# Optimization experiments

Hardware: AMD Instinct MI355X
Metric: run time of the kernel (lower is better)

## Reference

```python
import jax, jax.numpy as jnp
import numpy as np

D_MODEL = 512
NUM_HEADS = 8
D_K = D_MODEL // NUM_HEADS  # 64
NUM_FEATURES = 256
EPS = 1e-6


def _ortho_gaussian(m, d, seed):
    """Orthogonal random features: stacked QR blocks, rows rescaled to chi(d) norms."""
    rng = np.random.default_rng(seed)
    blocks = []
    for _ in range(int(np.ceil(m / d))):
        q, _ = np.linalg.qr(rng.standard_normal((d, d)))
        blocks.append(q.T)
    omega = np.concatenate(blocks, axis=0)[:m]
    norms = np.linalg.norm(rng.standard_normal((m, d)), axis=1)
    return (omega * norms[:, None]).astype(np.float32)


def setup_inputs() -> dict:
    key = jax.random.key(0)
    ks = jax.random.split(key, 7)
    B, L = 4, 8192
    s = 1.0 / np.sqrt(D_MODEL)
    return {
        "Q": jax.random.normal(ks[0], (B, L, D_MODEL), jnp.float32),
        "K": jax.random.normal(ks[1], (B, L, D_MODEL), jnp.float32),
        "V": jax.random.normal(ks[2], (B, L, D_MODEL), jnp.float32),
        "Wq": jax.random.normal(ks[3], (D_MODEL, D_MODEL), jnp.float32) * s,
        "Wk": jax.random.normal(ks[4], (D_MODEL, D_MODEL), jnp.float32) * s,
        "Wv": jax.random.normal(ks[5], (D_MODEL, D_MODEL), jnp.float32) * s,
        "Wo": jax.random.normal(ks[6], (D_MODEL, D_MODEL), jnp.float32) * s,
        "omega": jnp.asarray(_ortho_gaussian(NUM_FEATURES, D_K, 42)),
    }


def _phi(x, omega):
    """FAVOR+ positive softmax-kernel features. x: [B,H,L,d], omega: [m,d] -> [B,H,L,m]."""
    x = x * (D_K ** -0.25)  # fold in 1/sqrt(d_k) softmax scaling
    proj = jnp.einsum('bhld,md->bhlm', x, omega)
    sq = 0.5 * jnp.sum(x * x, axis=-1, keepdims=True)
    # subtract per-position max over features for numerical stability
    stab = jnp.max(proj, axis=-1, keepdims=True)
    return jnp.exp(proj - sq - stab) * (NUM_FEATURES ** -0.5) + EPS


def _split_heads(x, W):
    B, L, _ = x.shape
    return (x @ W).reshape(B, L, NUM_HEADS, D_K).transpose(0, 2, 1, 3)  # [B,H,L,d]


def reference(Q, K, V, Wq, Wk, Wv, Wo, omega):
    q = _split_heads(Q, Wq)
    k = _split_heads(K, Wk)
    v = _split_heads(V, Wv)
    qp = _phi(q, omega)  # [B,H,L,m]
    kp = _phi(k, omega)  # [B,H,L,m]
    # linear attention: O(L*m*d) instead of O(L^2)
    kv = jnp.einsum('bhlm,bhld->bhmd', kp, v)           # [B,H,m,d]
    num = jnp.einsum('bhlm,bhmd->bhld', qp, kv)          # [B,H,L,d]
    ksum = jnp.sum(kp, axis=2)                            # [B,H,m]
    den = jnp.einsum('bhlm,bhm->bhl', qp, ksum)          # [B,H,L]
    out = num / (den[..., None] + EPS)
    B, H, L, d = out.shape
    out = out.transpose(0, 2, 1, 3).reshape(B, L, H * d)
    return out @ Wo
```

## Files before the change

kernel.cpp:

```cpp
#include <hip/hip_runtime.h>

typedef unsigned int u32;
typedef __attribute__((ext_vector_type(8))) short short8;
typedef __attribute__((ext_vector_type(4))) short short4v;
typedef __attribute__((ext_vector_type(2))) u32 u32x2;
typedef __attribute__((ext_vector_type(4))) float f32x4;

#define DM 512
#define NH 8
#define DK 64
#define NF 256
#define L_ 8192
#define SCALE 0.35355339059327373f
#define INVSQM 0.0625f
#define EPS_ 1e-6f

__device__ __forceinline__ float bf2f(short s){
  union { u32 u; float f; } x; x.u = ((u32)(unsigned short)s) << 16; return x.f;
}
__device__ __forceinline__ short f2bf(float f){
  union { float f; u32 u; } x; x.f = f;
  u32 r = (x.u + 0x7FFF + ((x.u >> 16) & 1)) >> 16;
  return (short)r;
}
__device__ __forceinline__ u32 cvtpk(float lo, float hi){
  u32 r;
  asm("v_cvt_pk_bf16_f32 %0, %1, %2" : "=v"(r) : "v"(lo), "v"(hi));
  return r;
}

typedef const __attribute__((address_space(1))) u32* gas_t;
typedef __attribute__((address_space(3))) u32* las_t;
__device__ __forceinline__ void gl_lds16(const void* g, void* l){
  __builtin_amdgcn_global_load_lds((gas_t)g, (las_t)l, 16, 0, 0);
}
__device__ __forceinline__ f32x4 mfma16(short8 a, short8 b, f32x4 c){
  return __builtin_amdgcn_mfma_f32_16x16x32_bf16(a, b, c, 0, 0, 0);
}
__device__ __forceinline__ short8 lds_read8(const void* base, int byteoff){
  return *reinterpret_cast<const short8*>((const char*)base + byteoff);
}

__global__ __launch_bounds__(256) void k_wt(const float* __restrict__ W0, const float* __restrict__ W1,
                                            const float* __restrict__ W2, const float* __restrict__ W3,
                                            short* __restrict__ Wt){
  int bid = blockIdx.x;
  int mat = bid >> 6;
  int tr = (bid >> 3) & 7, tc = bid & 7;
  const float* W = mat==0 ? W0 : mat==1 ? W1 : mat==2 ? W2 : W3;
  short* O = Wt + (size_t)mat*DM*DM;
  __shared__ __align__(16) short tl[64*72];
  int t = threadIdx.x;
  #pragma unroll
  for (int i=0;i<4;++i){
    int c = i*256 + t;
    int r = c >> 4, cc = c & 15;
    f32x4 v = *reinterpret_cast<const f32x4*>(W + (size_t)(tr*64+r)*DM + tc*64 + cc*4);
    u32x2 o; o[0] = cvtpk(v[0], v[1]); o[1] = cvtpk(v[2], v[3]);
    *reinterpret_cast<u32x2*>((char*)tl + r*144 + cc*8) = o;
  }
  __syncthreads();
  #pragma unroll
  for (int i=0;i<2;++i){
    int c = i*256 + t;
    int n = c >> 3, kc = c & 7;
    short8 v;
    #pragma unroll
    for (int q=0;q<8;++q) v[q] = tl[(kc*8+q)*72 + n];
    *reinterpret_cast<short8*>(O + (size_t)(tc*64+n)*DM + tr*64 + kc*8) = v;
  }
}

__global__ __launch_bounds__(256) void k_omc(const float* __restrict__ Om, short* __restrict__ omc){
  int i = blockIdx.x*256 + threadIdx.x;
  f32x4 v = *((const f32x4*)Om + i);
  u32x2 o; o[0] = cvtpk(v[0], v[1]); o[1] = cvtpk(v[2], v[3]);
  *((u32x2*)omc + i) = o;
}

__global__ __launch_bounds__(256) void k_gemm3(const float* __restrict__ Q, const float* __restrict__ K,
                                               const float* __restrict__ V, const short* __restrict__ wt,
                                               short* __restrict__ qh, short* __restrict__ kh,
                                               short* __restrict__ vT, int rbase){
  __shared__ __align__(16) char smem[34816];
  short* lA = (short*)smem;
  short* lB = (short*)(smem + 16384);
  short* lC = (short*)smem;
  const int mode = blockIdx.y;
  const float* A = mode==0 ? Q : mode==1 ? K : V;
  const short* Bt = wt + (size_t)mode*DM*DM;
  const int t = threadIdx.x;
  const int w = t >> 6, lane = t & 63;
  const int wr = w >> 1, wc = w & 1;
  const int bid = blockIdx.x;
  const int bmx = gridDim.x >> 5;
  const int j = bid >> 3;
  const int bm = (bid & 7)*bmx + (j >> 2);
  const int bn = j & 3;
  const int row0 = bm*128, n0 = bn*128;
  f32x4 acc[4][4] = {};
  for (int ks=0; ks<8; ++ks){
    const float* gA32 = A + (size_t)(rbase+row0)*DM + ks*64;
    #pragma unroll
    for (int rnd=0; rnd<8; ++rnd){
      int c = rnd*256 + t;
      int r = c >> 4, cc = c & 15;
      f32x4 v = *reinterpret_cast<const f32x4*>(gA32 + (size_t)r*DM + cc*4);
      u32x2 o; o[0] = cvtpk(v[0], v[1]); o[1] = cvtpk(v[2], v[3]);
      int po = cc*8;
      *reinterpret_cast<u32x2*>((char*)lA + r*128 + (po ^ ((r&7)<<4))) = o;
    }
    const char* gB = (const char*)(Bt + (size_t)n0*DM + ks*64);
    #pragma unroll
    for (int rnd=0; rnd<4; ++rnd){
      int d = (rnd*256 + t)*16;
      int r = d >> 7, po = d & 127;
      gl_lds16(gB + (size_t)r*(DM*2) + (po ^ ((r&7)<<4)), (char*)lB + rnd*4096 + w*1024);
    }
    __syncthreads();
    #pragma unroll
    for (int kk=0; kk<2; ++kk){
      int kb = (kk*32 + ((lane>>4)<<3))*2;
      short8 af[4], bfr[4];
      #pragma unroll
      for (int i=0;i<4;++i){
        int m = wr*64 + i*16 + (lane&15);
        af[i] = lds_read8(lA, m*128 + (kb ^ ((m&7)<<4)));
      }
      #pragma unroll
      for (int j2=0;j2<4;++j2){
        int n = wc*64 + j2*16 + (lane&15);
        bfr[j2] = lds_read8(lB, n*128 + (kb ^ ((n&7)<<4)));
      }
      #pragma unroll
      for (int i=0;i<4;++i)
        #pragma unroll
        for (int j2=0;j2<4;++j2)
          acc[i][j2] = mfma16(af[i], bfr[j2], acc[i][j2]);
    }
    __syncthreads();
  }
  #pragma unroll
  for (int i=0;i<4;++i)
    #pragma unroll
    for (int j2=0;j2<4;++j2)
      #pragma unroll
      for (int jj=0;jj<4;++jj){
        int row = wr*64 + i*16 + ((lane>>4)<<2) + jj;
        int col = wc*64 + j2*16 + (lane&15);
        lC[row*136 + col] = f2bf(acc[i][j2][jj]);
      }
  __syncthreads();
  const int b = row0 >> 13;
  const int l0 = row0 & 8191;
  if (mode < 2){
    short* Os = mode ? kh : qh;
    #pragma unroll
    for (int it=0; it<8; ++it){
      int p = it*256 + t;
      int row = p >> 4, c16 = p & 15;
      short8 v = *reinterpret_cast<const short8*>((char*)lC + row*272 + c16*16);
      int col0 = n0 + c16*8;
      int h = col0 >> 6, dv = col0 & 63;
      size_t off = ((size_t)(b*NH + h)*L_ + (l0+row))*DK + dv;
      *reinterpret_cast<short8*>(Os + off) = v;
    }
  } else {
    #pragma unroll
    for (int it=0; it<8; ++it){
      int p = it*256 + t;
      int col = p >> 4, lp = p & 15;
      short8 v;
      #pragma unroll
      for (int q=0;q<8;++q) v[q] = lC[(lp*8+q)*136 + col];
      int h = (n0+col) >> 6, dv = (n0+col) & 63;
      size_t off = ((size_t)(b*NH+h)*DK + dv)*L_ + l0 + lp*8;
      *reinterpret_cast<short8*>(vT + off) = v;
    }
  }
}

__global__ __launch_bounds__(256) void k_gemmO(const short* __restrict__ A, const short* __restrict__ Bt,
                                               float* __restrict__ Out, int rbase){
  __shared__ __align__(16) short lA[128*64];
  __shared__ __align__(16) short lB[128*64];
  const int t = threadIdx.x;
  const int w = t >> 6, lane = t & 63;
  const int wr = w >> 1, wc = w & 1;
  const int bid = blockIdx.x;
  const int bmx = gridDim.x >> 5;
  const int j = bid >> 3;
  const int bm = (bid & 7)*bmx + (j >> 2);
  const int bn = j & 3;
  const int row0 = bm*128, n0 = bn*128;
  f32x4 acc[4][4] = {};
  for (int ks=0; ks<8; ++ks){
    const char* gA = (const char*)(A + (size_t)(rbase+row0)*DM + ks*64);
    #pragma unroll
    for (int rnd=0; rnd<4; ++rnd){
      int d = (rnd*256 + t)*16;
      int r = d >> 7, po = d & 127;
      gl_lds16(gA + (size_t)r*(DM*2) + (po ^ ((r&7)<<4)), (char*)lA + rnd*4096 + w*1024);
    }
    const char* gB = (const char*)(Bt + (size_t)n0*DM + ks*64);
    #pragma unroll
    for (int rnd=0; rnd<4; ++rnd){
      int d = (rnd*256 + t)*16;
      int r = d >> 7, po = d & 127;
      gl_lds16(gB + (size_t)r*(DM*2) + (po ^ ((r&7)<<4)), (char*)lB + rnd*4096 + w*1024);
    }
    __syncthreads();
    #pragma unroll
    for (int kk=0; kk<2; ++kk){
      int kb = (kk*32 + ((lane>>4)<<3))*2;
      short8 af[4], bfr[4];
      #pragma unroll
      for (int i=0;i<4;++i){
        int m = wr*64 + i*16 + (lane&15);
        af[i] = lds_read8(lA, m*128 + (kb ^ ((m&7)<<4)));
      }
      #pragma unroll
      for (int j2=0;j2<4;++j2){
        int n = wc*64 + j2*16 + (lane&15);
        bfr[j2] = lds_read8(lB, n*128 + (kb ^ ((n&7)<<4)));
      }
      #pragma unroll
      for (int i=0;i<4;++i)
        #pragma unroll
        for (int j2=0;j2<4;++j2)
          acc[i][j2] = mfma16(af[i], bfr[j2], acc[i][j2]);
    }
    __syncthreads();
  }
  #pragma unroll
  for (int i=0;i<4;++i)
    #pragma unroll
    for (int j2=0;j2<4;++j2)
      #pragma unroll
      for (int jj=0;jj<4;++jj){
        int row = wr*64 + i*16 + ((lane>>4)<<2) + jj;
        int col = wc*64 + j2*16 + (lane&15);
        Out[(size_t)(row0+row)*DM + n0 + col] = acc[i][j2][jj];
      }
}

__global__ __launch_bounds__(512) void k_phik(const short* __restrict__ kh, const short* __restrict__ vT,
                                              const short* __restrict__ omega,
                                              float* __restrict__ kvp, float* __restrict__ ksp){
  __shared__ __align__(16) short lOm[256*64];
  __shared__ __align__(16) short lK[128*64];
  __shared__ __align__(16) short lV[64*128];
  __shared__ __align__(16) short lP[256*136];
  __shared__ float lSq[128];
  __shared__ float lKsP[8][256];
  const int t = threadIdx.x, w = t>>6, lane = t&63;
  const int bid = blockIdx.x;
  const int bh = bid >> 3, sp = bid & 7;
  const char* khb = (const char*)(kh + (size_t)bh*L_*DK);
  const char* vtb = (const char*)(vT + (size_t)bh*DK*L_);
  #pragma unroll
  for (int rnd=0; rnd<4; ++rnd){
    int d = (rnd*512 + t)*16;
    int r = d >> 7, po = d & 127;
    gl_lds16((const char*)omega + r*128 + (po ^ ((r&7)<<4)), (char*)lOm + rnd*8192 + w*1024);
  }
  f32x4 kv[4][2] = {};
  float ksa[16] = {};
  for (int c=0;c<8;++c){
    int l0 = sp*1024 + c*128;
    #pragma unroll
    for (int rnd=0; rnd<2; ++rnd){
      int d = (rnd*512 + t)*16;
      { int r = d>>7, po = d&127;
        gl_lds16(khb + (size_t)(l0+r)*128 + (po ^ ((r&7)<<4)), (char*)lK + rnd*8192 + w*1024); }
      { int r = d>>8, po = d&255;
        gl_lds16(vtb + (size_t)r*(L_*2) + (size_t)l0*2 + (po ^ ((r&15)<<4)), (char*)lV + rnd*8192 + w*1024); }
    }
    __syncthreads();
    {
      int row = t >> 2, part = t & 3;
      float ss = 0.f;
      #pragma unroll
      for (int hh=0; hh<2; ++hh){
        int cb = part*32 + hh*16;
        short8 v = lds_read8(lK, row*128 + (cb ^ ((row&7)<<4)));
        #pragma unroll
        for (int q=0;q<8;++q){ float f = bf2f(v[q]); ss += f*f; }
      }
      ss += __shfl_xor(ss, 1, 64);
      ss += __shfl_xor(ss, 2, 64);
      if (part==0) lSq[row] = 0.0625f * ss;
    }
    __syncthreads();
    f32x4 p[16] = {};
    #pragma unroll
    for (int kk=0;kk<2;++kk){
      int kb = (kk*32 + ((lane>>4)<<3))*2;
      int m = w*16 + (lane&15);
      short8 a = lds_read8(lK, m*128 + (kb ^ ((m&7)<<4)));
      #pragma unroll
      for (int ft=0; ft<16; ++ft){
        int n = ft*16 + (lane&15);
        short8 b = lds_read8(lOm, n*128 + (kb ^ ((n&7)<<4)));
        p[ft] = mfma16(a, b, p[ft]);
      }
    }
    float mj[4] = {-1e30f,-1e30f,-1e30f,-1e30f};
    #pragma unroll
    for (int ft=0; ft<16; ++ft)
      #pragma unroll
      for (int j=0;j<4;++j){ float pv = p[ft][j]*SCALE; p[ft][j]=pv; mj[j] = fmaxf(mj[j], pv); }
    #pragma unroll
    for (int j=0;j<4;++j){
      float v = mj[j];
      v = fmaxf(v, __shfl_xor(v,1,64)); v = fmaxf(v, __shfl_xor(v,2,64));
      v = fmaxf(v, __shfl_xor(v,4,64)); v = fmaxf(v, __shfl_xor(v,8,64));
      mj[j] = v;
    }
    float sqv[4];
    #pragma unroll
    for (int j=0;j<4;++j) sqv[j] = lSq[w*16 + ((lane>>4)<<2) + j];
    int llb = w*16 + ((lane>>4)<<2);
    #pragma unroll
    for (int ft=0; ft<16; ++ft){
      int feat = ft*16 + (lane&15);
      float e0, e1, e2, e3;
      {
        e0 = __expf(p[ft][0] - sqv[0] - mj[0]) * INVSQM + EPS_;
        e1 = __expf(p[ft][1] - sqv[1] - mj[1]) * INVSQM + EPS_;
        e2 = __expf(p[ft][2] - sqv[2] - mj[2]) * INVSQM + EPS_;
        e3 = __expf(p[ft][3] - sqv[3] - mj[3]) * INVSQM + EPS_;
      }
      ksa[ft] += (e0 + e1) + (e2 + e3);
      u32x2 pk; pk[0] = cvtpk(e0, e1); pk[1] = cvtpk(e2, e3);
      *reinterpret_cast<u32x2*>((char*)lP + feat*272 + llb*2) = pk;
    }
    __syncthreads();
    #pragma unroll
    for (int ks2=0; ks2<4; ++ks2){
      int kb = (ks2*32 + ((lane>>4)<<3))*2;
      short8 a[4], b[2];
      #pragma unroll
      for (int i=0;i<4;++i){
        int m = i*16 + (lane&15);
        a[i] = lds_read8(lV, m*256 + (kb ^ ((m&15)<<4)));
      }
      #pragma unroll
      for (int j=0;j<2;++j){
        int n = (2*w+j)*16 + (lane&15);
        b[j] = lds_read8(lP, n*272 + kb);
      }
      #pragma unroll
      for (int i=0;i<4;++i)
        #pragma unroll
        for (int j=0;j<2;++j)
          kv[i][j] = mfma16(a[i], b[j], kv[i][j]);
    }
    __syncthreads();
  }
  float* kvb = kvp + (size_t)bid*64*256;
  #pragma unroll
  for (int i=0;i<4;++i)
    #pragma unroll
    for (int j=0;j<2;++j)
      #pragma unroll
      for (int jj=0;jj<4;++jj){
        int dv = i*16 + ((lane>>4)<<2) + jj;
        int feat = (2*w+j)*16 + (lane&15);
        kvb[dv*256 + feat] = kv[i][j][jj];
      }
  #pragma unroll
  for (int ft=0; ft<16; ++ft){
    float v = ksa[ft];
    v += __shfl_xor(v, 16, 64);
    v += __shfl_xor(v, 32, 64);
    if (lane < 16) lKsP[w][ft*16 + lane] = v;
  }
  __syncthreads();
  if (t < 256){
    float s = 0.f;
    #pragma unroll
    for (int wv=0; wv<8; ++wv) s += lKsP[wv][t];
    ksp[(size_t)bid*256 + t] = s;
  }
}

__global__ __launch_bounds__(256) void k_red(const float* __restrict__ kvp, const float* __restrict__ ksp,
                                             short* __restrict__ kvb, float* __restrict__ ksum){
  int bid = blockIdx.x;
  int bh = bid >> 3, part = bid & 7;
  int t = threadIdx.x;
  const float* base = kvp + (size_t)bh*8*16384;
  short* ob = kvb + (size_t)bh*16384;
  for (int i=0;i<8;++i){
    int e = part*2048 + i*256 + t;
    float s = 0.f;
    #pragma unroll
    for (int sp2=0; sp2<8; ++sp2) s += base[(size_t)sp2*16384 + e];
    ob[e] = f2bf(s);
  }
  if (part == 0){
    const float* kb = ksp + (size_t)bh*8*256;
    float s2 = 0.f;
    #pragma unroll
    for (int sp2=0; sp2<8; ++sp2) s2 += kb[sp2*256 + t];
    ksum[bh*256 + t] = s2;
  }
}

__global__ __launch_bounds__(512, 4) void k_phiq(const short* __restrict__ qh, const short* __restrict__ kvb,
                                                 const float* __restrict__ ksum, const short* __restrict__ omega,
                                                 short* __restrict__ attn){
  __shared__ __align__(16) char smem[69632];
  short* bufA = (short*)smem;
  short* bufB = (short*)(smem + 32768);
  float* lSq  = (float*)(smem + 67584);
  float* lKs  = (float*)(smem + 68096);
  float* lDen = (float*)(smem + 69120);
  const int t = threadIdx.x, w = t>>6, lane = t&63;
  const int bid = blockIdx.x;
  const int bh = bid >> 6, lt = bid & 63;
  const int l0 = lt*128;
  const char* qb = (const char*)(qh + (size_t)bh*L_*DK);
  #pragma unroll
  for (int rnd=0; rnd<4; ++rnd){
    int d = (rnd*512 + t)*16;
    int r = d>>7, po = d&127;
    gl_lds16((const char*)omega + r*128 + (po ^ ((r&7)<<4)), (char*)bufA + rnd*8192 + w*1024);
  }
  #pragma unroll
  for (int rnd=0; rnd<2; ++rnd){
    int d = (rnd*512 + t)*16;
    int r = d>>7, po = d&127;
    gl_lds16(qb + (size_t)(l0+r)*128 + (po ^ ((r&7)<<4)), (char*)bufB + rnd*8192 + w*1024);
  }
  if (t < 256) lKs[t] = ksum[bh*256 + t];
  __syncthreads();
  {
    int row = t >> 2, part = t & 3;
    float ss = 0.f;
    #pragma unroll
    for (int hh=0; hh<2; ++hh){
      int cb = part*32 + hh*16;
      short8 v = lds_read8(bufB, row*128 + (cb ^ ((row&7)<<4)));
      #pragma unroll
      for (int q=0;q<8;++q){ float f = bf2f(v[q]); ss += f*f; }
    }
    ss += __shfl_xor(ss, 1, 64);
    ss += __shfl_xor(ss, 2, 64);
    if (part==0) lSq[row] = 0.0625f * ss;
  }
  __syncthreads();
  f32x4 p[16] = {};
  #pragma unroll
  for (int kk=0;kk<2;++kk){
    int kb = (kk*32 + ((lane>>4)<<3))*2;
    int m = w*16 + (lane&15);
    short8 a = lds_read8(bufB, m*128 + (kb ^ ((m&7)<<4)));
    #pragma unroll
    for (int ft=0; ft<16; ++ft){
      int n = ft*16 + (lane&15);
      short8 b = lds_read8(bufA, n*128 + (kb ^ ((n&7)<<4)));
      p[ft] = mfma16(a, b, p[ft]);
    }
  }
  float mj[4] = {-1e30f,-1e30f,-1e30f,-1e30f};
  #pragma unroll
  for (int ft=0;ft<16;++ft)
    #pragma unroll
    for (int j=0;j<4;++j){ float pv = p[ft][j]*SCALE; p[ft][j]=pv; mj[j]=fmaxf(mj[j],pv); }
  #pragma unroll
  for (int j=0;j<4;++j){
    float v = mj[j];
    v = fmaxf(v,__shfl_xor(v,1,64)); v = fmaxf(v,__shfl_xor(v,2,64));
    v = fmaxf(v,__shfl_xor(v,4,64)); v = fmaxf(v,__shfl_xor(v,8,64));
    mj[j] = v;
  }
  float sqv[4];
  #pragma unroll
  for (int j=0;j<4;++j) sqv[j] = lSq[w*16 + ((lane>>4)<<2) + j];
  __syncthreads();
  const char* kvg = (const char*)(kvb + (size_t)bh*16384);
  #pragma unroll
  for (int rnd=0; rnd<4; ++rnd){
    int d = (rnd*512 + t)*16;
    int r = d>>9, po = d&511;
    gl_lds16(kvg + (size_t)r*512 + (po ^ ((r&31)<<4)), (char*)bufA + rnd*8192 + w*1024);
  }
  float dpart[4] = {0.f,0.f,0.f,0.f};
  const int rb = w*16 + ((lane>>4)<<2);
  #pragma unroll
  for (int ft=0;ft<8;++ft){
    int feat = ft*16 + (lane&15);
    float ksf = lKs[feat];
    #pragma unroll
    for (int j=0;j<4;++j){
      float e = __expf(p[ft][j]-sqv[j]-mj[j])*INVSQM + EPS_;
      dpart[j] += e*ksf;
      bufB[(rb+j)*136 + feat] = f2bf(e);
    }
  }
  __syncthreads();
  f32x4 nc[4] = {};
  #pragma unroll
  for (int ks2=0; ks2<4; ++ks2){
    int kb = (ks2*32 + ((lane>>4)<<3))*2;
    int n = w*16 + (lane&15);
    short8 bfr = lds_read8(bufB, n*272 + kb);
    #pragma unroll
    for (int i=0;i<4;++i){
      int mi = i*16 + (lane&15);
      short8 a = lds_read8(bufA, mi*512 + (kb ^ ((mi&31)<<4)));
      nc[i] = mfma16(a, bfr, nc[i]);
    }
  }
  #pragma unroll
  for (int ft=8;ft<16;++ft){
    int feat = ft*16 + (lane&15);
    float ksf = lKs[feat];
    #pragma unroll
    for (int j=0;j<4;++j){
      float e = __expf(p[ft][j]-sqv[j]-mj[j])*INVSQM + EPS_;
      dpart[j] += e*ksf;
      bufB[(rb+j)*136 + (feat-128)] = f2bf(e);
    }
  }
  #pragma unroll
  for (int j=0;j<4;++j){
    float v = dpart[j];
    v += __shfl_xor(v,1,64); v += __shfl_xor(v,2,64);
    v += __shfl_xor(v,4,64); v += __shfl_xor(v,8,64);
    if ((lane&15)==0) lDen[rb + j] = v;
  }
  #pragma unroll
  for (int ks2=4; ks2<8; ++ks2){
    int kbt = (ks2*32 + ((lane>>4)<<3))*2;
    int n = w*16 + (lane&15);
    short8 bfr = lds_read8(bufB, n*272 + (kbt - 256));
    #pragma unroll
    for (int i=0;i<4;++i){
      int mi = i*16 + (lane&15);
      short8 a = lds_read8(bufA, mi*512 + (kbt ^ ((mi&31)<<4)));
      nc[i] = mfma16(a, bfr, nc[i]);
    }
  }
  const int b = bh >> 3, h = bh & 7;
  const int l = w*16 + (lane&15);
  float rden = 1.0f / (lDen[l] + EPS_);
  #pragma unroll
  for (int i=0;i<4;++i){
    u32x2 ov;
    ov[0] = cvtpk(nc[i][0]*rden, nc[i][1]*rden);
    ov[1] = cvtpk(nc[i][2]*rden, nc[i][3]*rden);
    size_t off = ((size_t)(b*L_ + l0 + l))*DM + h*DK + i*16 + ((lane>>4)<<2);
    *reinterpret_cast<u32x2*>(attn + off) = ov;
  }
}

extern "C" void kernel_launch(void* const* d_in, const int* in_sizes, int n_in,
                              void* d_out, int out_size, void* d_ws, size_t ws_size,
                              hipStream_t stream){
  const float* Q  = (const float*)d_in[0];
  const float* K  = (const float*)d_in[1];
  const float* V  = (const float*)d_in[2];
  const float* Wq = (const float*)d_in[3];
  const float* Wk = (const float*)d_in[4];
  const float* Wv = (const float*)d_in[5];
  const float* Wo = (const float*)d_in[6];
  const float* Om = (const float*)d_in[7];
  char* ws = (char*)d_ws;

  short* wt  = (short*)(ws);
  short* omc = (short*)(ws + 2097152);

  k_wt<<<256, 256, 0, stream>>>(Wq, Wk, Wv, Wo, wt);
  k_omc<<<16, 256, 0, stream>>>(Om, omc);

  const size_t MONO_NEED = 120946688ull;
  if (ws_size >= MONO_NEED){
    short* qh   = (short*)(ws + 2162688);
    short* kh   = (short*)(ws + 35717120);
    short* vT   = (short*)(ws + 69271552);
    float* kvp  = (float*)(ws + 102825984);
    float* ksp  = (float*)(ws + 119603200);
    short* kvb  = (short*)(ws + 119865344);
    float* ksum = (float*)(ws + 120913920);
    short* attn = kh;
    k_gemm3<<<dim3(1024,3), 256, 0, stream>>>(Q, K, V, wt, qh, kh, vT, 0);
    k_phik<<<256, 512, 0, stream>>>(kh, vT, omc, kvp, ksp);
    k_red<<<256, 256, 0, stream>>>(kvp, ksp, kvb, ksum);
    k_phiq<<<2048, 512, 0, stream>>>(qh, kvb, ksum, omc, attn);
    k_gemmO<<<1024, 256, 0, stream>>>(attn, wt + 786432, (float*)d_out, 0);
  } else {
    short* qh   = (short*)(ws + 2162688);
    short* kh   = (short*)(ws + 10551296);
    short* vT   = (short*)(ws + 18939904);
    float* kvp  = (float*)(ws + 27328512);
    float* ksp  = (float*)(ws + 31522816);
    short* kvb  = (short*)(ws + 31588352);
    float* ksum = (float*)(ws + 31850496);
    short* attn = kh;
    for (int b=0; b<4; ++b){
      int rbase = b*8192;
      k_gemm3<<<dim3(256,3), 256, 0, stream>>>(Q, K, V, wt, qh, kh, vT, rbase);
      k_phik<<<64, 512, 0, stream>>>(kh, vT, omc, kvp, ksp);
      k_red<<<64, 256, 0, stream>>>(kvp, ksp, kvb, ksum);
      k_phiq<<<512, 512, 0, stream>>>(qh, kvb, ksum, omc, attn);
      k_gemmO<<<256, 256, 0, stream>>>(attn, wt + 786432,
                                       (float*)d_out + (size_t)b*8192*DM, 0);
    }
  }
}
```

Before: 269.7 us.

## Widen QKV projection tile to 128x256 to halve fp32 A reloads

The fused Q/K/V projection GEMM now computes a 128x256 output tile per block instead of 128x128, so each block converts and stages the fp32 activation tile once for twice as many output columns. The grid is halved, B staging doubles, accumulators double to 128 floats per thread, and the epilogue writes the two 128-column halves in sequence through a separate LDS region. The aim is to halve the redundant global reads and bf16 conversion of the large fp32 inputs. The cost is higher register and LDS use, which may lower occupancy, and fewer blocks in flight.

```diff
diff --git a/kernel.cpp b/kernel.cpp
--- a/kernel.cpp
+++ b/kernel.cpp
@@ -82,10 +82,10 @@
                                                const float* __restrict__ V, const short* __restrict__ wt,
                                                short* __restrict__ qh, short* __restrict__ kh,
                                                short* __restrict__ vT, int rbase){
-  __shared__ __align__(16) char smem[34816];
+  __shared__ __align__(16) char smem[51200];
   short* lA = (short*)smem;
   short* lB = (short*)(smem + 16384);
-  short* lC = (short*)smem;
+  short* lC = (short*)(smem + 16384);
   const int mode = blockIdx.y;
   const float* A = mode==0 ? Q : mode==1 ? K : V;
   const short* Bt = wt + (size_t)mode*DM*DM;
@@ -93,12 +93,12 @@
   const int w = t >> 6, lane = t & 63;
   const int wr = w >> 1, wc = w & 1;
   const int bid = blockIdx.x;
-  const int bmx = gridDim.x >> 5;
+  const int bmx = gridDim.x >> 4;
   const int j = bid >> 3;
-  const int bm = (bid & 7)*bmx + (j >> 2);
-  const int bn = j & 3;
-  const int row0 = bm*128, n0 = bn*128;
-  f32x4 acc[4][4] = {};
+  const int bm = (bid & 7)*bmx + (j >> 1);
+  const int bnp = j & 1;
+  const int row0 = bm*128, n0 = bnp*256;
+  f32x4 acc[2][4][4] = {};
   for (int ks=0; ks<8; ++ks){
     const float* gA32 = A + (size_t)(rbase+row0)*DM + ks*64;
     #pragma unroll
@@ -112,7 +112,7 @@
     }
     const char* gB = (const char*)(Bt + (size_t)n0*DM + ks*64);
     #pragma unroll
-    for (int rnd=0; rnd<4; ++rnd){
+    for (int rnd=0; rnd<8; ++rnd){
       int d = (rnd*256 + t)*16;
       int r = d >> 7, po = d & 127;
       gl_lds16(gB + (size_t)r*(DM*2) + (po ^ ((r&7)<<4)), (char*)lB + rnd*4096 + w*1024);
@@ -121,62 +121,72 @@
     #pragma unroll
     for (int kk=0; kk<2; ++kk){
       int kb = (kk*32 + ((lane>>4)<<3))*2;
-      short8 af[4], bfr[4];
+      short8 af[4];
       #pragma unroll
       for (int i=0;i<4;++i){
         int m = wr*64 + i*16 + (lane&15);
         af[i] = lds_read8(lA, m*128 + (kb ^ ((m&7)<<4)));
       }
       #pragma unroll
-      for (int j2=0;j2<4;++j2){
-        int n = wc*64 + j2*16 + (lane&15);
-        bfr[j2] = lds_read8(lB, n*128 + (kb ^ ((n&7)<<4)));
-      }
-      #pragma unroll
-      for (int i=0;i<4;++i)
+      for (int h=0;h<2;++h){
+        short8 bfr[4];
         #pragma unroll
-        for (int j2=0;j2<4;++j2)
-          acc[i][j2] = mfma16(af[i], bfr[j2], acc[i][j2]);
-    }
-    __syncthreads();
-  }
-  #pragma unroll
-  for (int i=0;i<4;++i)
-    #pragma unroll
-    for (int j2=0;j2<4;++j2)
-      #pragma unroll
-      for (int jj=0;jj<4;++jj){
-        int row = wr*64 + i*16 + ((lane>>4)<<2) + jj;
-        int col = wc*64 + j2*16 + (lane&15);
-        lC[row*136 + col] = f2bf(acc[i][j2][jj]);
-      }
-  __syncthreads();
+        for (int j2=0;j2<4;++j2){
+          int n = h*128 + wc*64 + j2*16 + (lane&15);
+          bfr[j2] = lds_read8(lB, n*128 + (kb ^ ((n&7)<<4)));
+        }
+        #pragma unroll
+        for (int i=0;i<4;++i)
+          #pragma unroll
+          for (int j2=0;j2<4;++j2)
+            acc[h][i][j2] = mfma16(af[i], bfr[j2], acc[h][i][j2]);
+      }
+    }
+    __syncthreads();
+  }
   const int b = row0 >> 13;
   const int l0 = row0 & 8191;
-  if (mode < 2){
-    short* Os = mode ? kh : qh;
-    #pragma unroll
-    for (int it=0; it<8; ++it){
-      int p = it*256 + t;
-      int row = p >> 4, c16 = p & 15;
-      short8 v = *reinterpret_cast<const short8*>((char*)lC + row*272 + c16*16);
-      int col0 = n0 + c16*8;
-      int h = col0 >> 6, dv = col0 & 63;
-      size_t off = ((size_t)(b*NH + h)*L_ + (l0+row))*DK + dv;
-      *reinterpret_cast<short8*>(Os + off) = v;
-    }
-  } else {
-    #pragma unroll
-    for (int it=0; it<8; ++it){
-      int p = it*256 + t;
-      int col = p >> 4, lp = p & 15;
-      short8 v;
-      #pragma unroll
-      for (int q=0;q<8;++q) v[q] = lC[(lp*8+q)*136 + col];
-      int h = (n0+col) >> 6, dv = (n0+col) & 63;
-      size_t off = ((size_t)(b*NH+h)*DK + dv)*L_ + l0 + lp*8;
-      *reinterpret_cast<short8*>(vT + off) = v;
-    }
+  #pragma unroll
+  for (int h=0;h<2;++h){
+    #pragma unroll
+    for (int i=0;i<4;++i)
+      #pragma unroll
+      for (int j2=0;j2<4;++j2)
+        #pragma unroll
+        for (int jj=0;jj<4;++jj){
+          int row = wr*64 + i*16 + ((lane>>4)<<2) + jj;
+          int col = wc*64 + j2*16 + (lane&15);
+          lC[row*136 + col] = f2bf(acc[h][i][j2][jj]);
+        }
+    __syncthreads();
+    const int colbase = n0 + h*128;
+    if (mode < 2){
+      short* Os = mode ? kh : qh;
+      #pragma unroll
+      for (int it=0; it<8; ++it){
+        int p = it*256 + t;
+        int row = p >> 4, c16 = p & 15;
+        short8 v = *reinterpret_cast<const short8*>((char*)lC + row*272 + c16*16);
+        int col0 = colbase + c16*8;
+        int hh = col0 >> 6, dv = col0 & 63;
+        size_t off = ((size_t)(b*NH + hh)*L_ + (l0+row))*DK + dv;
+        *reinterpret_cast<short8*>(Os + off) = v;
+      }
+    } else {
+      #pragma unroll
+      for (int it=0; it<8; ++it){
+        int p = it*256 + t;
+        int col = p >> 4, lp = p & 15;
+        short8 v;
+        #pragma unroll
+        for (int q=0;q<8;++q) v[q] = lC[(lp*8+q)*136 + col];
+        int ac = colbase + col;
+        int hh = ac >> 6, dv = ac & 63;
+        size_t off = ((size_t)(b*NH+hh)*DK + dv)*L_ + l0 + lp*8;
+        *reinterpret_cast<short8*>(vT + off) = v;
+      }
+    }
+    __syncthreads();
   }
 }
 
@@ -586,7 +596,7 @@
     short* kvb  = (short*)(ws + 119865344);
     float* ksum = (float*)(ws + 120913920);
     short* attn = kh;
-    k_gemm3<<<dim3(1024,3), 256, 0, stream>>>(Q, K, V, wt, qh, kh, vT, 0);
+    k_gemm3<<<dim3(512,3), 256, 0, stream>>>(Q, K, V, wt, qh, kh, vT, 0);
     k_phik<<<256, 512, 0, stream>>>(kh, vT, omc, kvp, ksp);
     k_red<<<256, 256, 0, stream>>>(kvp, ksp, kvb, ksum);
     k_phiq<<<2048, 512, 0, stream>>>(qh, kvb, ksum, omc, attn);
@@ -602,7 +612,7 @@
     short* attn = kh;
     for (int b=0; b<4; ++b){
       int rbase = b*8192;
-      k_gemm3<<<dim3(256,3), 256, 0, stream>>>(Q, K, V, wt, qh, kh, vT, rbase);
+      k_gemm3<<<dim3(128,3), 256, 0, stream>>>(Q, K, V, wt, qh, kh, vT, rbase);
       k_phik<<<64, 512, 0, stream>>>(kh, vT, omc, kvp, ksp);
       k_red<<<64, 256, 0, stream>>>(kvp, ksp, kvb, ksum);
       k_phiq<<<512, 512, 0, stream>>>(qh, kvb, ksum, omc, attn);
```

Result: no change. 273.7 us (+1.5%).
